# Optimization experiments

Measured on AMD Instinct MI355X. Metric: run time of the kernel, lower is better.

Reference implementation:

```python
import jax, jax.numpy as jnp
import numpy as np

N_QUBITS = 8
BATCH = 65536
PI = float(np.pi)


def rz_mat(t):
    # diag(e^{-i t/2}, e^{+i t/2}); t scalar or [B]
    t = jnp.asarray(t, jnp.float32).astype(jnp.complex64)
    e = jnp.exp(-0.5j * t)
    z = jnp.zeros_like(e)
    return jnp.stack([jnp.stack([e, z], -1), jnp.stack([z, jnp.conj(e)], -1)], -2)


def ry_mat(t):
    t = jnp.asarray(t, jnp.float32)
    c = jnp.cos(0.5 * t).astype(jnp.complex64)
    s = jnp.sin(0.5 * t).astype(jnp.complex64)
    return jnp.stack([jnp.stack([c, -s], -1), jnp.stack([s, c], -1)], -2)


def u3_mat(t, p, l):
    t = jnp.asarray(t, jnp.float32)
    c = jnp.cos(0.5 * t).astype(jnp.complex64)
    s = jnp.sin(0.5 * t).astype(jnp.complex64)
    ep = jnp.exp(1j * jnp.asarray(p, jnp.float32).astype(jnp.complex64))
    el = jnp.exp(1j * jnp.asarray(l, jnp.float32).astype(jnp.complex64))
    return jnp.stack([jnp.stack([c, -el * s], -1), jnp.stack([ep * s, ep * el * c], -1)], -2)


def apply_1q(state, U, w):
    # state: [B] + [2]*N_QUBITS; wire w is axis w+1 (wire 0 most significant, tq convention)
    s = jnp.moveaxis(state, w + 1, -1)
    if U.ndim == 3:  # batched gate (state prep with per-sample angles)
        s = jnp.einsum('b...i,bji->b...j', s, U)
    else:
        s = jnp.einsum('...i,ji->...j', s, U)
    return jnp.moveaxis(s, -1, w + 1)


def apply_cnot(state, c, t):
    s = jnp.moveaxis(state, (c + 1, t + 1), (-2, -1))
    s = jnp.concatenate([s[..., :1, :], s[..., 1:, ::-1]], axis=-2)
    return jnp.moveaxis(s, (-2, -1), (c + 1, t + 1))


def expval_z(state, w):
    p = jnp.square(jnp.abs(state))
    p = jnp.moveaxis(p, w + 1, 1).reshape(p.shape[0], 2, -1).sum(-1)
    return p[:, 0] - p[:, 1]


def build_state(x):
    # circuit_builder substitute: RY(theta), RZ(phi) on every qubit from |0...0>
    B = x.shape[0]
    theta, phi = x[:, 0], x[:, 1]
    state = jnp.zeros((B, 2 ** N_QUBITS), jnp.complex64).at[:, 0].set(1.0)
    state = state.reshape((B,) + (2,) * N_QUBITS)
    Ry, Rz = ry_mat(theta), rz_mat(phi)  # [B,2,2]
    for w in range(N_QUBITS):
        state = apply_1q(state, Ry, w)
        state = apply_1q(state, Rz, w)
    return state


def block(state, a, b, rzp, ry1p, ry2p, fin=None):
    # ZNOTY two-qubit convolution unitary on wires (a, b)
    fin = b if fin is None else fin
    state = apply_1q(state, rz_mat(-PI / 2), a)
    state = apply_cnot(state, a, b)
    state = apply_1q(state, rz_mat(rzp), b)
    state = apply_1q(state, ry_mat(ry1p), a)
    state = apply_cnot(state, b, a)
    state = apply_1q(state, ry_mat(ry2p), a)
    state = apply_cnot(state, a, b)
    state = apply_1q(state, rz_mat(PI / 2), fin)
    return state


def qcnn_forward(x, rz_params, ry_params, u3_params, W1, b1, W2, b2):
    s = build_state(x)
    # conv layer 1 (rz2, rz5, rz8, rz11 -> indices 1,4,7,10)
    s = block(s, 1, 0, rz_params[1], ry_params[0], ry_params[1])
    s = block(s, 3, 2, rz_params[4], ry_params[2], ry_params[3])
    s = block(s, 5, 4, rz_params[7], ry_params[4], ry_params[5])
    s = block(s, 7, 6, rz_params[10], ry_params[6], ry_params[7])
    # (mid-circuit expvals on [0,2,4,6] are non-destructive and discarded -> no state change)
    for i, w in enumerate([1, 3, 5, 7]):
        s = apply_1q(s, u3_mat(u3_params[i, 0], u3_params[i, 1], u3_params[i, 2]), w)
    # conv layer 2 (rz14, rz17, rz20 -> indices 13,16,19); (7,5) block's final fixed RZ
    # lands on wire 1 (as in the original source)
    s = block(s, 3, 1, rz_params[13], ry_params[8], ry_params[9])
    s = block(s, 7, 5, rz_params[16], ry_params[10], ry_params[11], fin=1)
    s = block(s, 5, 3, rz_params[19], ry_params[12], ry_params[13])
    s = apply_1q(s, u3_mat(u3_params[4, 0], u3_params[4, 1], u3_params[4, 2]), 3)
    s = apply_1q(s, u3_mat(u3_params[5, 0], u3_params[5, 1], u3_params[5, 2]), 7)
    feats = jnp.stack([expval_z(s, 3), expval_z(s, 7)], axis=-1)  # [B,2]
    h = jnp.tanh(feats @ W1 + b1)
    return jax.nn.sigmoid(h @ W2 + b2)  # [B,1]


def setup_inputs() -> dict:
    key = jax.random.key(0)
    ks = jax.random.split(key, 8)
    return {
        'x': jax.random.normal(ks[0], (BATCH, 2), jnp.float32),
        'rz_params': jax.random.normal(ks[1], (21,), jnp.float32),
        'ry_params': jax.random.normal(ks[2], (14,), jnp.float32),
        'u3_params': jax.random.normal(ks[3], (6, 3), jnp.float32),
        'W1': jax.random.normal(ks[4], (2, 10), jnp.float32) * 0.5,
        'b1': jax.random.normal(ks[5], (10,), jnp.float32) * 0.1,
        'W2': jax.random.normal(ks[6], (10, 1), jnp.float32) * 0.5,
        'b2': jax.random.normal(ks[7], (1,), jnp.float32) * 0.1,
    }


def reference(x, rz_params, ry_params, u3_params, W1, b1, W2, b2):
    return qcnn_forward(x, rz_params, ry_params, u3_params, W1, b1, W2, b2)
```

## Files before the change

### kernel.cpp

```cpp
#include <hip/hip_runtime.h>
#include <math.h>


#define QF 0.70710678118654752f

__device__ __forceinline__ float2 cmad2(float2 A, float2 a, float2 B, float2 b) {
  return make_float2(A.x*a.x - A.y*a.y + B.x*b.x - B.y*b.y,
                     A.x*a.y + A.y*a.x + B.x*b.y + B.y*b.x);
}

template<int CTRL>
__device__ __forceinline__ float dpps(float v) {
  int r = __builtin_amdgcn_update_dpp(__float_as_int(v), __float_as_int(v),
                                      CTRL, 0xF, 0xF, false);
  return __int_as_float(r);
}

template<int M>
__device__ __forceinline__ float lxs(float v, int lane) {
  if constexpr (M == 1)       return dpps<0xB1>(v);
  else if constexpr (M == 2)  return dpps<0x4E>(v);
  else if constexpr (M == 8)  return dpps<0x128>(v);
  else {
    int addr = (lane ^ M) << 2;
    return __int_as_float(__builtin_amdgcn_ds_bpermute(addr, __float_as_int(v)));
  }
}

template<int M>
__device__ __forceinline__ void xl8(const float2 (&z)[4], int lane,
                                    float (&px)[4], float (&py)[4]) {
#pragma unroll
  for (int j = 0; j < 4; ++j) px[j] = lxs<M>(z[j].x, lane);
#pragma unroll
  for (int j = 0; j < 4; ++j) py[j] = lxs<M>(z[j].y, lane);
}

template<int M>
__device__ __forceinline__ void rzdc(float2 (&z)[4], int lane, float c, float s) {
#pragma unroll
  for (int j = 0; j < 4; ++j) {
    bool hi;
    if constexpr (M < 64) hi = (lane & M) != 0;
    else                  hi = (j & (M >> 6)) != 0;
    float si = hi ? s : -s;
    z[j] = make_float2(c * z[j].x - si * z[j].y,
                       c * z[j].y + si * z[j].x);
  }
}

template<int M>
__device__ __forceinline__ void gate1r(float2 (&z)[4],
                                       float2 u00, float2 u01,
                                       float2 u10, float2 u11) {
  constexpr int jb = M >> 6;
#pragma unroll
  for (int j = 0; j < 4; ++j) {
    if ((j & jb) == 0) {
      float2 a = z[j], b = z[j + jb];
      z[j]      = cmad2(u00, a, u01, b);
      z[j + jb] = cmad2(u10, a, u11, b);
    }
  }
}

template<int M>
__device__ __forceinline__ void gate1c(float2 (&z)[4], int lane,
                                       float2 u00, float2 u01,
                                       float2 u10, float2 u11) {
  float px[4], py[4];
  xl8<M>(z, lane, px, py);
  bool hi = (lane & M) != 0;
  float2 A = hi ? u11 : u00;
  float2 B = hi ? u10 : u01;
#pragma unroll
  for (int j = 0; j < 4; ++j)
    z[j] = cmad2(A, z[j], B, make_float2(px[j], py[j]));
}

template<int M>
__device__ __forceinline__ void rygc(float2 (&z)[4], int lane, float c, float s) {
  if constexpr (M < 64) {
    float px[4], py[4];
    xl8<M>(z, lane, px, py);
    float sg = (lane & M) ? s : -s;
#pragma unroll
    for (int j = 0; j < 4; ++j)
      z[j] = make_float2(c * z[j].x + sg * px[j], c * z[j].y + sg * py[j]);
  } else {
    gate1r<M>(z, make_float2(c, 0.f), make_float2(-s, 0.f),
                 make_float2(s, 0.f), make_float2(c, 0.f));
  }
}

template<int M>
__device__ __forceinline__ void u3c(float2 (&z)[4], int lane,
                                    float2 u00, float2 u01,
                                    float2 u10, float2 u11) {
  if constexpr (M < 64) gate1c<M>(z, lane, u00, u01, u10, u11);
  else                  gate1r<M>(z, u00, u01, u10, u11);
}

template<int MC, int MT>
__device__ __forceinline__ void cnotg(float2 (&z)[4], int lane) {
  if constexpr (MT < 64) {
    float px[4], py[4];
#pragma unroll
    for (int j = 0; j < 4; ++j) {
      constexpr bool dummy = true; (void)dummy;
      if ((MC < 64) || (((j << 6) & MC) != 0))
        px[j] = lxs<MT>(z[j].x, lane);
    }
#pragma unroll
    for (int j = 0; j < 4; ++j) {
      if ((MC < 64) || (((j << 6) & MC) != 0))
        py[j] = lxs<MT>(z[j].y, lane);
    }
#pragma unroll
    for (int j = 0; j < 4; ++j) {
      if ((MC < 64) || (((j << 6) & MC) != 0)) {
        bool sel = (MC >= 64) || ((lane & MC) != 0);
        z[j].x = sel ? px[j] : z[j].x;
        z[j].y = sel ? py[j] : z[j].y;
      }
    }
  } else {
    constexpr int jb = MT >> 6;
#pragma unroll
    for (int j = 0; j < 4; ++j) {
      if ((j & jb) == 0) {
        if (MC >= 64) {
          constexpr int cjb = MC >> 6;
          if ((j & cjb) != 0) { float2 t = z[j]; z[j] = z[j + jb]; z[j + jb] = t; }
        } else {
          bool sel = (lane & MC) != 0;
          float2 a = z[j], b = z[j + jb];
          z[j]      = make_float2(sel ? b.x : a.x, sel ? b.y : a.y);
          z[j + jb] = make_float2(sel ? a.x : b.x, sel ? a.y : b.y);
        }
      }
    }
  }
}

template<int MA, int MB, int MF>
__device__ __forceinline__ void blockgc(float2 (&z)[4], int lane,
                                        float2 zc, float2 y1, float2 y2) {
  rzdc<MA>(z, lane, QF, -QF);
  cnotg<MA, MB>(z, lane);
  rzdc<MB>(z, lane, zc.x, zc.y);
  rygc<MA>(z, lane, y1.x, y1.y);
  cnotg<MB, MA>(z, lane);
  rygc<MA>(z, lane, y2.x, y2.y);
  cnotg<MA, MB>(z, lane);
  rzdc<MF>(z, lane, QF, QF);
}

__device__ __forceinline__ float fast_tanh(float x) {
  float e = __expf(2.f * x);
  return 1.f - 2.f / (e + 1.f);
}

__device__ __forceinline__ float rlane(float v, int l) {
  return __int_as_float(__builtin_amdgcn_readlane(__float_as_int(v), l));
}

__device__ __forceinline__ void wsum4u(float& a, float& b, float& c, float& d,
                                       int lane) {
  a += lxs<1>(a, lane);  b += lxs<1>(b, lane);
  c += lxs<1>(c, lane);  d += lxs<1>(d, lane);
  a += lxs<2>(a, lane);  b += lxs<2>(b, lane);
  c += lxs<2>(c, lane);  d += lxs<2>(d, lane);
  a += lxs<4>(a, lane);  b += lxs<4>(b, lane);
  c += lxs<4>(c, lane);  d += lxs<4>(d, lane);
  a += lxs<8>(a, lane);  b += lxs<8>(b, lane);
  c += lxs<8>(c, lane);  d += lxs<8>(d, lane);
  a += lxs<16>(a, lane); b += lxs<16>(b, lane);
  c += lxs<16>(c, lane); d += lxs<16>(d, lane);
  a = rlane(a, 0) + rlane(a, 32);
  b = rlane(b, 0) + rlane(b, 32);
  c = rlane(c, 0) + rlane(c, 32);
  d = rlane(d, 0) + rlane(d, 32);
}

__global__ __launch_bounds__(64)
void qcnn_sim(const float* __restrict__ rz, const float* __restrict__ ry,
              const float* __restrict__ u3, float2* __restrict__ G) {
  int lane = threadIdx.x;
  int p = blockIdx.x;

  float rzl[21], ryl[14], u3l[18];
#pragma unroll
  for (int k = 0; k < 21; ++k) rzl[k] = rz[k];
#pragma unroll
  for (int k = 0; k < 14; ++k) ryl[k] = ry[k];
#pragma unroll
  for (int k = 0; k < 18; ++k) u3l[k] = u3[k];

  float2 brz[7], by1[7], by2[7];
#pragma unroll
  for (int i = 0; i < 7; ++i) {
    __sincosf(0.5f * rzl[3*i+1], &brz[i].y, &brz[i].x);
    __sincosf(0.5f * ryl[2*i],   &by1[i].y, &by1[i].x);
    __sincosf(0.5f * ryl[2*i+1], &by2[i].y, &by2[i].x);
  }
  float2 U00[6], U01[6], U10[6], U11[6];
#pragma unroll
  for (int g = 0; g < 6; ++g) {
    float s, c;   __sincosf(0.5f * u3l[3*g], &s, &c);
    float sp, cp; __sincosf(u3l[3*g+1], &sp, &cp);
    float sl, cl; __sincosf(u3l[3*g+2], &sl, &cl);
    float spl, cpl; __sincosf(u3l[3*g+1] + u3l[3*g+2], &spl, &cpl);
    U00[g] = make_float2(c, 0.f);
    U01[g] = make_float2(-cl * s, -sl * s);
    U10[g] = make_float2(cp * s, sp * s);
    U11[g] = make_float2(cpl * c, spl * c);
  }

  float2 z[4];
#pragma unroll
  for (int j = 0; j < 4; ++j) {
    int k = (j << 6) | lane;
    z[j] = make_float2(__popc(k) == p ? 1.f : 0.f, 0.f);
  }

  blockgc<1, 8, 8>(z, lane, brz[0], by1[0], by2[0]);
  blockgc<64, 4, 4>(z, lane, brz[1], by1[1], by2[1]);
  blockgc<128, 16, 16>(z, lane, brz[2], by1[2], by2[2]);
  blockgc<2, 32, 32>(z, lane, brz[3], by1[3], by2[3]);
  u3c<1>(z, lane, U00[0], U01[0], U10[0], U11[0]);
  u3c<64>(z, lane, U00[1], U01[1], U10[1], U11[1]);
  u3c<128>(z, lane, U00[2], U01[2], U10[2], U11[2]);
  u3c<2>(z, lane, U00[3], U01[3], U10[3], U11[3]);
  blockgc<64, 1, 1>(z, lane, brz[4], by1[4], by2[4]);
  blockgc<2, 128, 1>(z, lane, brz[5], by1[5], by2[5]);
  blockgc<128, 64, 64>(z, lane, brz[6], by1[6], by2[6]);
  u3c<64>(z, lane, U00[4], U01[4], U10[4], U11[4]);
  u3c<2>(z, lane, U00[5], U01[5], U10[5], U11[5]);

#pragma unroll
  for (int j = 0; j < 4; ++j)
    G[p * 256 + (j << 6) + lane] = z[j];
}

__global__ __launch_bounds__(256)
void qcnn_eval(const float* __restrict__ x, const float2* __restrict__ G,
               const float* __restrict__ W1, const float* __restrict__ b1,
               const float* __restrict__ W2, const float* __restrict__ b2,
               float* __restrict__ out, int B) {
  __shared__ float2 gl[9 * 256];
  __shared__ float4 stab[45];
  int tid = threadIdx.x;
  int wid = tid >> 6, lane = tid & 63;

  int i = blockIdx.x * 256 + tid;
  float2 tp = reinterpret_cast<const float2*>(x)[i < B ? i : 0];

  float W1l[20], b1l[10], W2l[10], b2l;
#pragma unroll
  for (int k = 0; k < 20; ++k) W1l[k] = W1[k];
#pragma unroll
  for (int k = 0; k < 10; ++k) b1l[k] = b1[k];
#pragma unroll
  for (int k = 0; k < 10; ++k) W2l[k] = W2[k];
  b2l = b2[0];

#pragma unroll
  for (int w = 0; w < 9; ++w)
    gl[w * 256 + tid] = G[w * 256 + tid];

  float th = tp.x, ph = tp.y;
  float stt, ct;
  __sincosf(0.5f * th, &stt, &ct);
  float c1, s1;
  __sincosf(ph, &s1, &c1);

  __syncthreads();

  float z7 = (lane & 2) ? -1.f : 1.f;
  for (int pr = wid; pr < 45; pr += 4) {
    int pp = 0, base = 0, s = pr;
    while (s >= base + 9 - pp) { base += 9 - pp; ++pp; }
    int qq = pp + (s - base);

    float Ar = 0.f, Ai = 0.f, Br = 0.f, Bi = 0.f;
#pragma unroll
    for (int m = 0; m < 4; ++m) {
      float2 a = gl[pp * 256 + (m << 6) + lane];
      float2 b = gl[qq * 256 + (m << 6) + lane];
      float cr = a.x * b.x + a.y * b.y;
      float ci = a.x * b.y - a.y * b.x;
      if (m & 1) { Br += cr; Bi += ci; } else { Ar += cr; Ai += ci; }
    }
    float v0 = Ar - Br;
    float v1 = Ai - Bi;
    float v2 = z7 * (Ar + Br);
    float v3 = z7 * (Ai + Bi);
    wsum4u(v0, v1, v2, v3, lane);
    if (lane == 0) {
      float sc = (pp == qq) ? 1.f : 2.f;
      stab[pr] = make_float4(sc * v0, sc * v1, sc * v2, sc * v3);
    }
  }
  __syncthreads();

  if (i >= B) return;

  float cpw[17], spw[17];
  cpw[0] = 1.f; spw[0] = 1.f;
#pragma unroll
  for (int k = 1; k < 17; ++k) { cpw[k] = cpw[k-1] * ct; spw[k] = spw[k-1] * stt; }

  float cd[9], sd[9];
  cd[0] = 1.f; sd[0] = 0.f;
  cd[1] = c1;  sd[1] = s1;
#pragma unroll
  for (int d = 2; d < 9; ++d) {
    cd[d] = cd[d-1] * c1 - sd[d-1] * s1;
    sd[d] = sd[d-1] * c1 + cd[d-1] * s1;
  }

  float f3 = 0.f, f7 = 0.f;
  int sidx = 0;
#pragma unroll
  for (int pp = 0; pp < 9; ++pp) {
#pragma unroll
    for (int qq = pp; qq < 9; ++qq) {
      float4 s4 = stab[sidx]; ++sidx;
      float w = cpw[16 - pp - qq] * spw[pp + qq];
      int d = qq - pp;
      f3 += w * (s4.x * cd[d] - s4.y * sd[d]);
      f7 += w * (s4.z * cd[d] - s4.w * sd[d]);
    }
  }

  float acc = b2l;
#pragma unroll
  for (int j = 0; j < 10; ++j) {
    float h = fast_tanh(f3 * W1l[j] + f7 * W1l[10 + j] + b1l[j]);
    acc += h * W2l[j];
  }
  out[i] = 1.f / (1.f + __expf(-acc));
}

extern "C" void kernel_launch(void* const* d_in, const int* in_sizes, int n_in,
                              void* d_out, int out_size, void* d_ws, size_t ws_size,
                              hipStream_t stream) {
  const float* x  = (const float*)d_in[0];
  const float* rz = (const float*)d_in[1];
  const float* ry = (const float*)d_in[2];
  const float* u3 = (const float*)d_in[3];
  const float* W1 = (const float*)d_in[4];
  const float* b1 = (const float*)d_in[5];
  const float* W2 = (const float*)d_in[6];
  const float* b2 = (const float*)d_in[7];

  float2* G = (float2*)d_ws;

  qcnn_sim<<<9, 64, 0, stream>>>(rz, ry, u3, G);

  int B = in_sizes[0] / 2;
  qcnn_eval<<<(B + 255) / 256, 256, 0, stream>>>(x, G, W1, b1, W2, b2,
                                                 (float*)d_out, B);
}
```

Measured before the change: 19.67 us.

## Compute Gram-table inner products per lane instead of per-pair wave reductions

The 45 pairwise inner products of precomputed gate columns were each computed by one wave with a cross-lane DPP/readlane reduction. Now each lane owns one pair and sums serially over a 64-element segment per wave. A second pass adds the four wave partials through shared memory. The shared buffer stride is padded to 257 to avoid bank conflicts on these strided reads. This removes long cross-lane reduction chains at the cost of an extra barrier, idle lanes (45 of 64), and a different sign/ordering mapping that must match the old z7 and parity split.

Result: faster. 16.52 us (-16.0%).

```diff
diff --git a/kernel.cpp b/kernel.cpp
--- a/kernel.cpp
+++ b/kernel.cpp
@@ -3,6 +3,7 @@
 
 
 #define QF 0.70710678118654752f
+#define GSTR 257
 
 __device__ __forceinline__ float2 cmad2(float2 A, float2 a, float2 B, float2 b) {
   return make_float2(A.x*a.x - A.y*a.y + B.x*b.x - B.y*b.y,
@@ -106,16 +107,11 @@
   if constexpr (MT < 64) {
     float px[4], py[4];
 #pragma unroll
-    for (int j = 0; j < 4; ++j) {
-      constexpr bool dummy = true; (void)dummy;
-      if ((MC < 64) || (((j << 6) & MC) != 0))
-        px[j] = lxs<MT>(z[j].x, lane);
-    }
-#pragma unroll
-    for (int j = 0; j < 4; ++j) {
-      if ((MC < 64) || (((j << 6) & MC) != 0))
-        py[j] = lxs<MT>(z[j].y, lane);
-    }
+    for (int j = 0; j < 4; ++j)
+      if ((MC < 64) || (((j << 6) & MC) != 0)) px[j] = lxs<MT>(z[j].x, lane);
+#pragma unroll
+    for (int j = 0; j < 4; ++j)
+      if ((MC < 64) || (((j << 6) & MC) != 0)) py[j] = lxs<MT>(z[j].y, lane);
 #pragma unroll
     for (int j = 0; j < 4; ++j) {
       if ((MC < 64) || (((j << 6) & MC) != 0)) {
@@ -159,28 +155,6 @@
 __device__ __forceinline__ float fast_tanh(float x) {
   float e = __expf(2.f * x);
   return 1.f - 2.f / (e + 1.f);
-}
-
-__device__ __forceinline__ float rlane(float v, int l) {
-  return __int_as_float(__builtin_amdgcn_readlane(__float_as_int(v), l));
-}
-
-__device__ __forceinline__ void wsum4u(float& a, float& b, float& c, float& d,
-                                       int lane) {
-  a += lxs<1>(a, lane);  b += lxs<1>(b, lane);
-  c += lxs<1>(c, lane);  d += lxs<1>(d, lane);
-  a += lxs<2>(a, lane);  b += lxs<2>(b, lane);
-  c += lxs<2>(c, lane);  d += lxs<2>(d, lane);
-  a += lxs<4>(a, lane);  b += lxs<4>(b, lane);
-  c += lxs<4>(c, lane);  d += lxs<4>(d, lane);
-  a += lxs<8>(a, lane);  b += lxs<8>(b, lane);
-  c += lxs<8>(c, lane);  d += lxs<8>(d, lane);
-  a += lxs<16>(a, lane); b += lxs<16>(b, lane);
-  c += lxs<16>(c, lane); d += lxs<16>(d, lane);
-  a = rlane(a, 0) + rlane(a, 32);
-  b = rlane(b, 0) + rlane(b, 32);
-  c = rlane(c, 0) + rlane(c, 32);
-  d = rlane(d, 0) + rlane(d, 32);
 }
 
 __global__ __launch_bounds__(64)
@@ -243,12 +217,19 @@
     G[p * 256 + (j << 6) + lane] = z[j];
 }
 
+__device__ __forceinline__ void tdec(int idx, int& pp, int& qq) {
+  int base = 0; pp = 0;
+  while (idx >= base + 9 - pp) { base += 9 - pp; ++pp; }
+  qq = pp + (idx - base);
+}
+
 __global__ __launch_bounds__(256)
 void qcnn_eval(const float* __restrict__ x, const float2* __restrict__ G,
                const float* __restrict__ W1, const float* __restrict__ b1,
                const float* __restrict__ W2, const float* __restrict__ b2,
                float* __restrict__ out, int B) {
-  __shared__ float2 gl[9 * 256];
+  __shared__ float2 gl[9 * GSTR];
+  __shared__ float4 part[4][45];
   __shared__ float4 stab[45];
   int tid = threadIdx.x;
   int wid = tid >> 6, lane = tid & 63;
@@ -267,7 +248,7 @@
 
 #pragma unroll
   for (int w = 0; w < 9; ++w)
-    gl[w * 256 + tid] = G[w * 256 + tid];
+    gl[w * GSTR + tid] = G[w * 256 + tid];
 
   float th = tp.x, ph = tp.y;
   float stt, ct;
@@ -277,30 +258,38 @@
 
   __syncthreads();
 
-  float z7 = (lane & 2) ? -1.f : 1.f;
-  for (int pr = wid; pr < 45; pr += 4) {
-    int pp = 0, base = 0, s = pr;
-    while (s >= base + 9 - pp) { base += 9 - pp; ++pp; }
-    int qq = pp + (s - base);
-
-    float Ar = 0.f, Ai = 0.f, Br = 0.f, Bi = 0.f;
-#pragma unroll
-    for (int m = 0; m < 4; ++m) {
-      float2 a = gl[pp * 256 + (m << 6) + lane];
-      float2 b = gl[qq * 256 + (m << 6) + lane];
-      float cr = a.x * b.x + a.y * b.y;
-      float ci = a.x * b.y - a.y * b.x;
-      if (m & 1) { Br += cr; Bi += ci; } else { Ar += cr; Ai += ci; }
-    }
-    float v0 = Ar - Br;
-    float v1 = Ai - Bi;
-    float v2 = z7 * (Ar + Br);
-    float v3 = z7 * (Ai + Bi);
-    wsum4u(v0, v1, v2, v3, lane);
-    if (lane == 0) {
-      float sc = (pp == qq) ? 1.f : 2.f;
-      stab[pr] = make_float4(sc * v0, sc * v1, sc * v2, sc * v3);
-    }
+  if (lane < 45) {
+    int pp, qq; tdec(lane, pp, qq);
+    const float2* rp = &gl[pp * GSTR + (wid << 6)];
+    const float2* rq = &gl[qq * GSTR + (wid << 6)];
+    float pr_ = 0.f, pi_ = 0.f, mr_ = 0.f, mi_ = 0.f;
+#pragma unroll
+    for (int kk = 0; kk < 64; kk += 4) {
+#pragma unroll
+      for (int u = 0; u < 4; ++u) {
+        float2 a = rp[kk + u];
+        float2 b = rq[kk + u];
+        float cr = a.x * b.x + a.y * b.y;
+        float ci = a.x * b.y - a.y * b.x;
+        if (u < 2) { pr_ += cr; pi_ += ci; }
+        else       { mr_ += cr; mi_ += ci; }
+      }
+    }
+    float s3w = (wid & 1) ? -1.f : 1.f;
+    part[wid][lane] = make_float4(s3w * (pr_ + mr_), s3w * (pi_ + mi_),
+                                  pr_ - mr_, pi_ - mi_);
+  }
+  __syncthreads();
+
+  if (tid < 45) {
+    int pp, qq; tdec(tid, pp, qq);
+    float4 p0 = part[0][tid], p1 = part[1][tid];
+    float4 p2 = part[2][tid], p3 = part[3][tid];
+    float sc = (pp == qq) ? 1.f : 2.f;
+    stab[tid] = make_float4(sc * (p0.x + p1.x + p2.x + p3.x),
+                            sc * (p0.y + p1.y + p2.y + p3.y),
+                            sc * (p0.z + p1.z + p2.z + p3.z),
+                            sc * (p0.w + p1.w + p2.w + p3.w));
   }
   __syncthreads();
 
```
